# Performance work log

Measured on AMD Instinct MI355X. Metric: run time of the kernel, lower is better.

Reference implementation:

```python
import jax, jax.numpy as jnp
import numpy as np

ALPHA = 0.2  # leaky relu slope
NEG_INF = -9e15  # matches torch constant -9000000000000000.0


def setup_inputs() -> dict:
    key = jax.random.key(0)
    k1, k2, k3, k4, k5 = jax.random.split(key, 5)
    B, S, FIN, FOUT, H = 1, 4096, 128, 64, 8
    input_seq = jax.random.normal(k1, (B, S, FIN), dtype=jnp.float32)
    adj = jax.random.randint(k2, (B, S, S), 0, 2, dtype=jnp.int32)
    W = jax.random.normal(k3, (H, FIN, FOUT), dtype=jnp.float32) * 0.1
    a_1 = jax.random.normal(k4, (H, FOUT, 1), dtype=jnp.float32) * 0.1
    a_2 = jax.random.normal(k5, (H, FOUT, 1), dtype=jnp.float32) * 0.1
    return {"input_seq": input_seq, "adj": adj, "W": W, "a_1": a_1, "a_2": a_2}


def reference(input_seq, adj, W, a_1, a_2):
    B, S, _ = input_seq.shape
    H, _, FOUT = W.shape
    # h: [B, H, S, FOUT]
    h = jnp.einsum('bni,hio->bhno', input_seq, W)
    f1 = jnp.einsum('bhno,hoz->bhnz', h, a_1)[..., 0]  # [B,H,S]
    f2 = jnp.einsum('bhno,hoz->bhnz', h, a_2)[..., 0]  # [B,H,S]
    # e[b,h,i,j] = f1[i] + f2[j]
    e = jax.nn.leaky_relu(f1[:, :, :, None] + f2[:, :, None, :], ALPHA)
    mask = adj[:, None, :, :] > 0  # [B,1,S,S] broadcast over heads
    e = jnp.where(mask, e, NEG_INF)
    # NOTE: original softmax is over dim=2 (source-node axis), not -1
    attention = jax.nn.softmax(e, axis=2)
    # dropout is inference-mode no-op
    node_out = jnp.einsum('bhij,bhjo->bhio', attention, h)  # [B,H,S,FOUT]
    node_out = jnp.transpose(node_out, (0, 2, 1, 3)).reshape(B, S, H * FOUT)
    node_out = jax.nn.elu(node_out)
    return jnp.squeeze(node_out)
```

## Files before the change

### kernel.cpp

```cpp
#include <hip/hip_runtime.h>

#define S 4096
#define PS 4128
#define FIN 128
#define FOUT 64
#define H 8
#define ALPHA 0.2f

typedef __attribute__((ext_vector_type(2)))  _Float16 f16x2;
typedef __attribute__((ext_vector_type(8)))  _Float16 f16x8;
typedef __attribute__((ext_vector_type(16))) float    f32x16;

__device__ __forceinline__ unsigned short f2h(float x) {
    return __builtin_bit_cast(unsigned short, (_Float16)x);
}

__global__ __launch_bounds__(256) void k_proj(const float* __restrict__ X,
                                              const float* __restrict__ W,
                                              const float* __restrict__ a1,
                                              const float* __restrict__ a2,
                                              unsigned short* __restrict__ hT,
                                              float2* __restrict__ E1h,
                                              float2* __restrict__ E2p) {
    __shared__ float xs[64][36];
    __shared__ float Ws[32][68];
    const int h  = blockIdx.y;
    const int j0 = blockIdx.x * 64;
    const int t  = threadIdx.x;
    const int fg = t & 15, rg = t >> 4;
    const int jr = t >> 2, q = t & 3;
    const int kw = t >> 3, cw = t & 7;
    float acc[4][4] = {};
#pragma unroll
    for (int k0 = 0; k0 < FIN; k0 += 32) {
        *(float4*)&xs[jr][q * 8]      = *(const float4*)&X[(j0 + jr) * FIN + k0 + q * 8];
        *(float4*)&xs[jr][q * 8 + 4]  = *(const float4*)&X[(j0 + jr) * FIN + k0 + q * 8 + 4];
        *(float4*)&Ws[kw][cw * 8]     = *(const float4*)&W[(h * FIN + k0 + kw) * FOUT + cw * 8];
        *(float4*)&Ws[kw][cw * 8 + 4] = *(const float4*)&W[(h * FIN + k0 + kw) * FOUT + cw * 8 + 4];
        __syncthreads();
#pragma unroll
        for (int kc = 0; kc < 8; ++kc) {
            float4 xr[4], wr[4];
#pragma unroll
            for (int r = 0; r < 4; ++r) xr[r] = *(const float4*)&xs[4 * rg + r][kc * 4];
#pragma unroll
            for (int kk = 0; kk < 4; ++kk) wr[kk] = *(const float4*)&Ws[kc * 4 + kk][fg * 4];
#pragma unroll
            for (int r = 0; r < 4; ++r) {
                const float* xp = (const float*)&xr[r];
#pragma unroll
                for (int kk = 0; kk < 4; ++kk) {
                    const float xv = xp[kk];
                    acc[r][0] += xv * wr[kk].x;
                    acc[r][1] += xv * wr[kk].y;
                    acc[r][2] += xv * wr[kk].z;
                    acc[r][3] += xv * wr[kk].w;
                }
            }
        }
        __syncthreads();
    }
    const float4 a1v = *(const float4*)&a1[h * FOUT + fg * 4];
    const float4 a2v = *(const float4*)&a2[h * FOUT + fg * 4];
#pragma unroll
    for (int r = 0; r < 4; ++r) {
        float p1 = acc[r][0] * a1v.x + acc[r][1] * a1v.y + acc[r][2] * a1v.z + acc[r][3] * a1v.w;
        float p2 = acc[r][0] * a2v.x + acc[r][1] * a2v.y + acc[r][2] * a2v.z + acc[r][3] * a2v.w;
#pragma unroll
        for (int off = 1; off < 16; off <<= 1) {
            p1 += __shfl_xor(p1, off, 64);
            p2 += __shfl_xor(p2, off, 64);
        }
        if (fg == 0) {
            const int row = j0 + 4 * rg + r;
            E1h[(size_t)row * H + h] = make_float2(__expf(p1), __expf(ALPHA * p1));
            E2p[h * S + row]         = make_float2(__expf(p2), __expf(ALPHA * p2));
        }
    }
#pragma unroll
    for (int c = 0; c < 4; ++c) {
        ushort4 pk;
        pk.x = f2h(acc[0][c]);
        pk.y = f2h(acc[1][c]);
        pk.z = f2h(acc[2][c]);
        pk.w = f2h(acc[3][c]);
        *(ushort4*)&hT[(size_t)(h * FOUT + fg * 4 + c) * PS + j0 + 4 * rg] = pk;
    }
}

__global__ __launch_bounds__(256) void k_colsum(const int* __restrict__ adj,
                                                const float2* __restrict__ E1h,
                                                const float2* __restrict__ E2p,
                                                float* __restrict__ Dpart,
                                                unsigned int* __restrict__ bmT) {
    __shared__ float red[4][H][64];
    const int j0    = blockIdx.x * 64;
    const int ibase = blockIdx.y * 256;
    const int t  = threadIdx.x;
    const int jl = t & 63;
    const int wv = __builtin_amdgcn_readfirstlane(t >> 6);
    float2 e2v[H];
    float Dl[H];
#pragma unroll
    for (int hh = 0; hh < H; ++hh) { e2v[hh] = E2p[hh * S + j0 + jl]; Dl[hh] = 0.f; }
    const int rowbase = ibase + wv * 64;
    for (int s = 0; s < 64; ++s) {
        const int row = rowbase + s;
        const float2* __restrict__ e1r = E1h + (size_t)row * H;
        const int av = adj[(size_t)row * S + j0 + jl];
        const unsigned long long blt = __ballot(av != 0);
        if (jl == 0) {
            bmT[(j0 >> 5) * S + row]       = (unsigned int)blt;
            bmT[((j0 >> 5) + 1) * S + row] = (unsigned int)(blt >> 32);
        }
        const float bf = av != 0 ? 1.f : 0.f;
#pragma unroll
        for (int hh = 0; hh < H; ++hh) {
            const float2 e1 = e1r[hh];
            Dl[hh] = fmaf(bf, fmaxf(e1.x * e2v[hh].x, e1.y * e2v[hh].y), Dl[hh]);
        }
    }
#pragma unroll
    for (int hh = 0; hh < H; ++hh) red[wv][hh][jl] = Dl[hh];
    __syncthreads();
    if (wv == 0) {
#pragma unroll
        for (int hh = 0; hh < H; ++hh) {
            const float sum = red[0][hh][jl] + red[1][hh][jl] +
                              red[2][hh][jl] + red[3][hh][jl];
            Dpart[(blockIdx.y * H + hh) * S + j0 + jl] = sum;
        }
    }
}

__global__ __launch_bounds__(256) void k_finish(const float* __restrict__ Dpart,
                                                const float2* __restrict__ E2p,
                                                uint2* __restrict__ wE2h) {
    const int idx = blockIdx.x * 256 + threadIdx.x;
    const int hh = idx >> 11, pp = idx & 2047;
    const int j = 2 * pp;
    float sx = 0.f, sy = 0.f;
#pragma unroll
    for (int z = 0; z < 16; ++z) {
        const float2 d = *(const float2*)&Dpart[(z * H + hh) * S + j];
        sx += d.x; sy += d.y;
    }
    const float4 e2 = *(const float4*)&E2p[hh * S + j];
    const float wa = 1.0f / sx, wb = 1.0f / sy;
    f16x2 qx, qy;
    qx[0] = (_Float16)(e2.x * wa); qx[1] = (_Float16)(e2.z * wb);
    qy[0] = (_Float16)(e2.y * wa); qy[1] = (_Float16)(e2.w * wb);
    wE2h[idx] = make_uint2(__builtin_bit_cast(unsigned int, qx),
                           __builtin_bit_cast(unsigned int, qy));
}

__global__ __launch_bounds__(512, 6) void k_attn(const unsigned int* __restrict__ bmT,
                                                 const float2* __restrict__ E1h,
                                                 const uint2* __restrict__ wE2h,
                                                 const unsigned short* __restrict__ hT,
                                                 float* __restrict__ outp) {
    __shared__ __align__(16) char smem[36864];
    const int h  = blockIdx.y;
    const int i0 = blockIdx.x * 64;
    const int z  = blockIdx.z;
    const int t  = threadIdx.x;

    uint2* wE2s = (uint2*)smem;
    ((uint4*)wE2s)[t] = ((const uint4*)(wE2h + h * (S / 2) + z * 1024))[t];
    __syncthreads();

    const int lane = t & 63, wv = t >> 6;
    const int q = wv >> 1, mw = wv & 1;
    const int am = lane & 31, kh = lane >> 5;
    const int i  = i0 + mw * 32 + am;
    const int jbase = z * 2048 + q * 512;

    const float2 e1 = E1h[(size_t)i * H + h];
    f16x2 ea2, eb2;
    ea2[0] = ea2[1] = (_Float16)e1.x;
    eb2[0] = eb2[1] = (_Float16)e1.y;

    f32x16 acc0 = {0,0,0,0,0,0,0,0,0,0,0,0,0,0,0,0};
    f32x16 acc1 = {0,0,0,0,0,0,0,0,0,0,0,0,0,0,0,0};

    const unsigned short* b0p = hT + (size_t)(h * FOUT + am) * PS + jbase;
    const unsigned short* b1p = hT + (size_t)(h * FOUT + am + 32) * PS + jbase;
    const unsigned int* bmcol = bmT + (jbase >> 5) * S + i;
    const uint2* e2s = wE2s + q * 256 + kh * 4;
    const unsigned int sh = kh * 8;

    for (int jt = 0; jt < 8; ++jt) {
        const unsigned int w0 = bmcol[(2 * jt) * S];
        const unsigned int w1 = bmcol[(2 * jt + 1) * S];
        unsigned int bys[4];
        bys[0] = (w0 >> sh) & 0xffu;
        bys[1] = (w0 >> (sh + 16)) & 0xffu;
        bys[2] = (w1 >> sh) & 0xffu;
        bys[3] = (w1 >> (sh + 16)) & 0xffu;
#pragma unroll
        for (int s = 0; s < 4; ++s) {
            const int ko = jt * 64 + s * 16 + kh * 8;
            const f16x8 b0 = *(const f16x8*)(b0p + ko);
            const f16x8 b1 = *(const f16x8*)(b1p + ko);
            const uint4 eA = *(const uint4*)(e2s + jt * 32 + s * 8);
            const uint4 eB = *(const uint4*)(e2s + jt * 32 + s * 8 + 2);
            const unsigned int by = bys[s];
            uint4 aw;
#define GAT_PAIR(pp, qxu, qyu, dst)                                               \
            {                                                                     \
                const f16x2 pa = ea2 * __builtin_bit_cast(f16x2, qxu);            \
                const f16x2 pb = eb2 * __builtin_bit_cast(f16x2, qyu);            \
                const unsigned int pm = __builtin_bit_cast(unsigned int,          \
                    __builtin_elementwise_max(pa, pb));                           \
                const unsigned int t2 = (by >> (2 * pp)) & 3u;                    \
                const unsigned int msk = ((0u - (t2 & 1u)) & 0xFFFFu) |           \
                                         ((0u - (t2 >> 1)) << 16);                \
                dst = pm & msk;                                                   \
            }
            GAT_PAIR(0, eA.x, eA.y, aw.x)
            GAT_PAIR(1, eA.z, eA.w, aw.y)
            GAT_PAIR(2, eB.x, eB.y, aw.z)
            GAT_PAIR(3, eB.z, eB.w, aw.w)
#undef GAT_PAIR
            const f16x8 a = __builtin_bit_cast(f16x8, aw);
            acc0 = __builtin_amdgcn_mfma_f32_32x32x16_f16(a, b0, acc0, 0, 0, 0);
            acc1 = __builtin_amdgcn_mfma_f32_32x32x16_f16(a, b1, acc1, 0, 0, 0);
        }
    }
    __syncthreads();

    float* r1 = (float*)smem;
    float* r3 = (float*)(smem + 18432);
    const int ro = (mw * 64 + lane) * 36;
    if (q == 1) {
#pragma unroll
        for (int r = 0; r < 16; ++r) { r1[ro + r] = acc0[r]; r1[ro + 16 + r] = acc1[r]; }
    }
    if (q == 3) {
#pragma unroll
        for (int r = 0; r < 16; ++r) { r3[ro + r] = acc0[r]; r3[ro + 16 + r] = acc1[r]; }
    }
    __syncthreads();
    if (q == 0) {
#pragma unroll
        for (int r = 0; r < 16; ++r) { acc0[r] += r1[ro + r]; acc1[r] += r1[ro + 16 + r]; }
    }
    if (q == 2) {
#pragma unroll
        for (int r = 0; r < 16; ++r) { acc0[r] += r3[ro + r]; acc1[r] += r3[ro + 16 + r]; }
    }
    __syncthreads();
    if (q == 2) {
#pragma unroll
        for (int r = 0; r < 16; ++r) { r1[ro + r] = acc0[r]; r1[ro + 16 + r] = acc1[r]; }
    }
    __syncthreads();
    if (q == 0) {
#pragma unroll
        for (int r = 0; r < 16; ++r) { acc0[r] += r1[ro + r]; acc1[r] += r1[ro + 16 + r]; }
        float* dst = outp + (size_t)z * (S * H * FOUT);
#pragma unroll
        for (int r = 0; r < 16; ++r) {
            const int il  = (r & 3) + 8 * (r >> 2) + 4 * kh;
            const int row = i0 + mw * 32 + il;
            dst[row * (H * FOUT) + h * FOUT + am]      = acc0[r];
            dst[row * (H * FOUT) + h * FOUT + 32 + am] = acc1[r];
        }
    }
}

__global__ __launch_bounds__(256) void k_elu(const float* __restrict__ outp,
                                             float* __restrict__ out) {
    const int idx = (blockIdx.x * 256 + threadIdx.x) * 4;
    const float4 p0 = *(const float4*)&outp[idx];
    const float4 p1 = *(const float4*)&outp[S * H * FOUT + idx];
    float4 v;
    v.x = p0.x + p1.x; v.y = p0.y + p1.y; v.z = p0.z + p1.z; v.w = p0.w + p1.w;
    v.x = v.x > 0.f ? v.x : __expf(v.x) - 1.f;
    v.y = v.y > 0.f ? v.y : __expf(v.y) - 1.f;
    v.z = v.z > 0.f ? v.z : __expf(v.z) - 1.f;
    v.w = v.w > 0.f ? v.w : __expf(v.w) - 1.f;
    *(float4*)&out[idx] = v;
}

extern "C" void kernel_launch(void* const* d_in, const int* in_sizes, int n_in,
                              void* d_out, int out_size, void* d_ws, size_t ws_size,
                              hipStream_t stream) {
    const float* X   = (const float*)d_in[0];
    const int*   adj = (const int*)d_in[1];
    const float* W   = (const float*)d_in[2];
    const float* a1  = (const float*)d_in[3];
    const float* a2  = (const float*)d_in[4];
    float* out = (float*)d_out;

    char* ws = (char*)d_ws;
    unsigned short* hT   = (unsigned short*)ws;
    float2*         E1h  = (float2*)(ws + 4325376);
    float2*         E2p  = (float2*)(ws + 4587520);
    float*          Dpart= (float*)(ws + 4849664);
    unsigned int*   bmT  = (unsigned int*)(ws + 6946816);
    uint2*          wE2h = (uint2*)(ws + 9043968);
    float*          outp = (float*)(ws + 9175040);

    k_proj  <<<dim3(S / 64, H),       256, 0, stream>>>(X, W, a1, a2, hT, E1h, E2p);
    k_colsum<<<dim3(S / 64, S / 256), 256, 0, stream>>>(adj, E1h, E2p, Dpart, bmT);
    k_finish<<<dim3(H * S / 512),     256, 0, stream>>>(Dpart, E2p, wE2h);
    k_attn  <<<dim3(S / 64, H, 2),    512, 0, stream>>>(bmT, E1h, wE2h, hT, outp);
    k_elu   <<<dim3(S * H * FOUT / 1024), 256, 0, stream>>>(outp, out);
}
```

Before: 209.6 us.

## Stage hT tiles in swizzled LDS with double buffering and wider row tiles

The attention kernel now covers 128 rows per block using four row-waves and two K-split groups. hT B-tiles are staged through XOR-swizzled, double-buffered shared memory, and the next tile plus the mask words are prefetched into registers, so four waves share each global load. The cross-wave reduction shrinks to a single exchange and the mask is applied by an f16 multiply instead of bit ops. In exchange it adds a barrier per iteration, uses more LDS and lowers the occupancy hint.

New measurement: 191.4 us. -8.6%, faster.

```diff
diff --git a/kernel.cpp b/kernel.cpp
--- a/kernel.cpp
+++ b/kernel.cpp
@@ -154,26 +154,26 @@
                            __builtin_bit_cast(unsigned int, qy));
 }
 
-__global__ __launch_bounds__(512, 6) void k_attn(const unsigned int* __restrict__ bmT,
+__global__ __launch_bounds__(512, 4) void k_attn(const unsigned int* __restrict__ bmT,
                                                  const float2* __restrict__ E1h,
                                                  const uint2* __restrict__ wE2h,
                                                  const unsigned short* __restrict__ hT,
                                                  float* __restrict__ outp) {
-    __shared__ __align__(16) char smem[36864];
+    __shared__ __align__(16) char smem[40960];
     const int h  = blockIdx.y;
-    const int i0 = blockIdx.x * 64;
+    const int i0 = blockIdx.x * 128;
     const int z  = blockIdx.z;
     const int t  = threadIdx.x;
 
-    uint2* wE2s = (uint2*)smem;
+    uint2* wE2s = (uint2*)(smem + 32768);
     ((uint4*)wE2s)[t] = ((const uint4*)(wE2h + h * (S / 2) + z * 1024))[t];
-    __syncthreads();
 
     const int lane = t & 63, wv = t >> 6;
-    const int q = wv >> 1, mw = wv & 1;
+    const int q  = wv >> 2;
+    const int mw = wv & 3;
     const int am = lane & 31, kh = lane >> 5;
     const int i  = i0 + mw * 32 + am;
-    const int jbase = z * 2048 + q * 512;
+    const int jbase = z * 2048 + q * 1024;
 
     const float2 e1 = E1h[(size_t)i * H + h];
     f16x2 ea2, eb2;
@@ -183,25 +183,41 @@
     f32x16 acc0 = {0,0,0,0,0,0,0,0,0,0,0,0,0,0,0,0};
     f32x16 acc1 = {0,0,0,0,0,0,0,0,0,0,0,0,0,0,0,0};
 
-    const unsigned short* b0p = hT + (size_t)(h * FOUT + am) * PS + jbase;
-    const unsigned short* b1p = hT + (size_t)(h * FOUT + am + 32) * PS + jbase;
+    const int tq = t & 255;
+    const int sf = tq >> 2;
+    const int c0 = tq & 3;
+    unsigned short* Bq = (unsigned short*)smem + q * 8192;
+    const unsigned short* hstage = hT + (size_t)(h * FOUT + sf) * PS + jbase;
+
     const unsigned int* bmcol = bmT + (jbase >> 5) * S + i;
-    const uint2* e2s = wE2s + q * 256 + kh * 4;
+    const uint2* e2s = wE2s + q * 512 + kh * 4;
     const unsigned int sh = kh * 8;
 
-    for (int jt = 0; jt < 8; ++jt) {
-        const unsigned int w0 = bmcol[(2 * jt) * S];
-        const unsigned int w1 = bmcol[(2 * jt + 1) * S];
+    uint4 va = *(const uint4*)(hstage + c0 * 8);
+    uint4 vb = *(const uint4*)(hstage + 32 + c0 * 8);
+    unsigned int bw0 = bmcol[0];
+    unsigned int bw1 = bmcol[S];
+    __syncthreads();
+
+    for (int jt = 0; jt < 16; ++jt) {
+        unsigned short* Bc = Bq + (jt & 1) * 4096;
+        *(uint4*)&Bc[sf * 64 + ((c0 ^ (sf & 7)) * 8)]       = va;
+        *(uint4*)&Bc[sf * 64 + (((c0 + 4) ^ (sf & 7)) * 8)] = vb;
+        const unsigned int m0 = bw0, m1 = bw1;
+        __syncthreads();
+        if (jt < 15) {
+            va  = *(const uint4*)(hstage + (jt + 1) * 64 + c0 * 8);
+            vb  = *(const uint4*)(hstage + (jt + 1) * 64 + 32 + c0 * 8);
+            bw0 = bmcol[(2 * jt + 2) * S];
+            bw1 = bmcol[(2 * jt + 3) * S];
+        }
         unsigned int bys[4];
-        bys[0] = (w0 >> sh) & 0xffu;
-        bys[1] = (w0 >> (sh + 16)) & 0xffu;
-        bys[2] = (w1 >> sh) & 0xffu;
-        bys[3] = (w1 >> (sh + 16)) & 0xffu;
+        bys[0] = (m0 >> sh) & 0xffu;
+        bys[1] = (m0 >> (sh + 16)) & 0xffu;
+        bys[2] = (m1 >> sh) & 0xffu;
+        bys[3] = (m1 >> (sh + 16)) & 0xffu;
 #pragma unroll
         for (int s = 0; s < 4; ++s) {
-            const int ko = jt * 64 + s * 16 + kh * 8;
-            const f16x8 b0 = *(const f16x8*)(b0p + ko);
-            const f16x8 b1 = *(const f16x8*)(b1p + ko);
             const uint4 eA = *(const uint4*)(e2s + jt * 32 + s * 8);
             const uint4 eB = *(const uint4*)(e2s + jt * 32 + s * 8 + 2);
             const unsigned int by = bys[s];
@@ -210,19 +226,22 @@
             {                                                                     \
                 const f16x2 pa = ea2 * __builtin_bit_cast(f16x2, qxu);            \
                 const f16x2 pb = eb2 * __builtin_bit_cast(f16x2, qyu);            \
-                const unsigned int pm = __builtin_bit_cast(unsigned int,          \
-                    __builtin_elementwise_max(pa, pb));                           \
-                const unsigned int t2 = (by >> (2 * pp)) & 3u;                    \
-                const unsigned int msk = ((0u - (t2 & 1u)) & 0xFFFFu) |           \
-                                         ((0u - (t2 >> 1)) << 16);                \
-                dst = pm & msk;                                                   \
+                const f16x2 pm = __builtin_elementwise_max(pa, pb);               \
+                const unsigned int b2 = (by >> (2 * pp)) & 3u;                    \
+                const unsigned int vv = (b2 | (b2 << 15)) & 0x00010001u;          \
+                const unsigned int mm = (vv << 14) - (vv << 10);    \
+                dst = __builtin_bit_cast(unsigned int,                            \
+                      pm * __builtin_bit_cast(f16x2, mm));                        \
             }
             GAT_PAIR(0, eA.x, eA.y, aw.x)
             GAT_PAIR(1, eA.z, eA.w, aw.y)
             GAT_PAIR(2, eB.x, eB.y, aw.z)
             GAT_PAIR(3, eB.z, eB.w, aw.w)
 #undef GAT_PAIR
-            const f16x8 a = __builtin_bit_cast(f16x8, aw);
+            const int chunk = s * 2 + kh;
+            const f16x8 a  = __builtin_bit_cast(f16x8, aw);
+            const f16x8 b0 = *(const f16x8*)&Bc[am * 64 + ((chunk ^ (am & 7)) * 8)];
+            const f16x8 b1 = *(const f16x8*)&Bc[(am + 32) * 64 + ((chunk ^ ((am + 32) & 7)) * 8)];
             acc0 = __builtin_amdgcn_mfma_f32_32x32x16_f16(a, b0, acc0, 0, 0, 0);
             acc1 = __builtin_amdgcn_mfma_f32_32x32x16_f16(a, b1, acc1, 0, 0, 0);
         }
@@ -230,27 +249,8 @@
     __syncthreads();
 
     float* r1 = (float*)smem;
-    float* r3 = (float*)(smem + 18432);
     const int ro = (mw * 64 + lane) * 36;
     if (q == 1) {
-#pragma unroll
-        for (int r = 0; r < 16; ++r) { r1[ro + r] = acc0[r]; r1[ro + 16 + r] = acc1[r]; }
-    }
-    if (q == 3) {
-#pragma unroll
-        for (int r = 0; r < 16; ++r) { r3[ro + r] = acc0[r]; r3[ro + 16 + r] = acc1[r]; }
-    }
-    __syncthreads();
-    if (q == 0) {
-#pragma unroll
-        for (int r = 0; r < 16; ++r) { acc0[r] += r1[ro + r]; acc1[r] += r1[ro + 16 + r]; }
-    }
-    if (q == 2) {
-#pragma unroll
-        for (int r = 0; r < 16; ++r) { acc0[r] += r3[ro + r]; acc1[r] += r3[ro + 16 + r]; }
-    }
-    __syncthreads();
-    if (q == 2) {
 #pragma unroll
         for (int r = 0; r < 16; ++r) { r1[ro + r] = acc0[r]; r1[ro + 16 + r] = acc1[r]; }
     }
@@ -305,6 +305,6 @@
     k_proj  <<<dim3(S / 64, H),       256, 0, stream>>>(X, W, a1, a2, hT, E1h, E2p);
     k_colsum<<<dim3(S / 64, S / 256), 256, 0, stream>>>(adj, E1h, E2p, Dpart, bmT);
     k_finish<<<dim3(H * S / 512),     256, 0, stream>>>(Dpart, E2p, wE2h);
-    k_attn  <<<dim3(S / 64, H, 2),    512, 0, stream>>>(bmT, E1h, wE2h, hT, outp);
+    k_attn  <<<dim3(S / 128, H, 2),   512, 0, stream>>>(bmT, E1h, wE2h, hT, outp);
     k_elu   <<<dim3(S * H * FOUT / 1024), 256, 0, stream>>>(outp, out);
 }
```
